# Kernel tuning notes

Measured on AMD Instinct MI355X. Metric: run time of the kernel, lower is better.

## Reference

```python
import jax, jax.numpy as jnp
import numpy as np

EPS = 1e-5

def maxpool2(x):
    # 2x2 max pool, stride 2, NCHW
    B, C, H, W = x.shape
    return x.reshape(B, C, H // 2, 2, W // 2, 2).max(axis=(3, 5))

def conv1x1(x, w, b):
    # x: [B,C,H,W], w: [O,C], b: [O]
    return jnp.einsum('bchw,oc->bohw', x, w) + b[None, :, None, None]

def setup_inputs() -> dict:
    key = jax.random.key(0)
    ks = jax.random.split(key, 12)
    B, C, IC, H, W = 8, 256, 128, 128, 128
    s = 0.05
    return {
        'rgb': jax.random.normal(ks[0], (B, C, H, W), jnp.float32),
        'event': jax.random.normal(ks[1], (B, C, H, W), jnp.float32),
        'g_w': jax.random.normal(ks[2], (IC, C), jnp.float32) * s,
        'g_b': jax.random.normal(ks[3], (IC,), jnp.float32) * s,
        'theta_w': jax.random.normal(ks[4], (IC, C), jnp.float32) * s,
        'theta_b': jax.random.normal(ks[5], (IC,), jnp.float32) * s,
        'phi_w': jax.random.normal(ks[6], (IC, C), jnp.float32) * s,
        'phi_b': jax.random.normal(ks[7], (IC,), jnp.float32) * s,
        'W_w': jax.random.normal(ks[8], (C, IC), jnp.float32) * s,
        'W_b': jax.random.normal(ks[9], (C,), jnp.float32) * s,
        'bn_gamma': jax.random.normal(ks[10], (C,), jnp.float32) * s + 1.0,
        'bn_beta': jax.random.normal(ks[11], (C,), jnp.float32) * s,
    }

def reference(rgb, event, g_w, g_b, theta_w, theta_b, phi_w, phi_b, W_w, W_b, bn_gamma, bn_beta):
    B = rgb.shape[0]
    IC = g_w.shape[0]
    # initial shared 2x2 max pool on both modalities
    rgb_p = maxpool2(rgb)      # [B,C,h2,w2]
    ev_p = maxpool2(event)
    h2, w2 = rgb_p.shape[2], rgb_p.shape[3]
    # projections; g and phi have an extra sub_sample pool
    g_x = maxpool2(conv1x1(ev_p, g_w, g_b)).reshape(B, IC, -1)      # [B,IC,Nkv]
    g_x = jnp.swapaxes(g_x, 1, 2)                                    # [B,Nkv,IC]
    theta_x = conv1x1(rgb_p, theta_w, theta_b).reshape(B, IC, -1)    # [B,IC,Nq]
    theta_x = jnp.swapaxes(theta_x, 1, 2)                            # [B,Nq,IC]
    phi_x = maxpool2(conv1x1(ev_p, phi_w, phi_b)).reshape(B, IC, -1) # [B,IC,Nkv]
    # full attention: scores -> softmax -> value matmul
    f = jnp.einsum('bqc,bck->bqk', theta_x, phi_x)                   # [B,Nq,Nkv]
    f_div_C = jax.nn.softmax(f, axis=-1)
    y = jnp.einsum('bqk,bkc->bqc', f_div_C, g_x)                     # [B,Nq,IC]
    y = jnp.swapaxes(y, 1, 2).reshape(B, IC, h2, w2)
    # output 1x1 conv + BatchNorm (training-mode batch stats, biased var)
    W_y = conv1x1(y, W_w, W_b)                                       # [B,C,h2,w2]
    mean = W_y.mean(axis=(0, 2, 3), keepdims=True)
    var = W_y.var(axis=(0, 2, 3), keepdims=True)
    W_y = (W_y - mean) * jax.lax.rsqrt(var + EPS)
    W_y = W_y * bn_gamma[None, :, None, None] + bn_beta[None, :, None, None]
    z = W_y + rgb_p
    z = jnp.repeat(jnp.repeat(z, 2, axis=2), 2, axis=3)
    return z
```

## Files before the change

### kernel.cpp

```cpp
#include <hip/hip_runtime.h>
#include <stdint.h>


typedef unsigned short u16;
typedef short bf16x8 __attribute__((ext_vector_type(8)));
typedef float f32x4 __attribute__((ext_vector_type(4)));

#define MFMA16(a, b, c) __builtin_amdgcn_mfma_f32_16x16x32_bf16(a, b, c, 0, 0, 0)

__device__ __forceinline__ u16 f2bf(float x) {
    union { float f; unsigned int u; } v; v.f = x;
    unsigned int u = v.u;
    unsigned int r = u + 0x7fffu + ((u >> 16) & 1u);
    return (u16)(r >> 16);
}
__device__ __forceinline__ float bf2f(u16 h) {
    union { unsigned int u; float f; } v; v.u = ((unsigned int)h) << 16;
    return v.f;
}

__global__ void wsplit_kernel(const float* __restrict__ tw, const float* __restrict__ pw,
                              const float* __restrict__ gw, const float* __restrict__ ww,
                              u16* __restrict__ planes, float* __restrict__ acc) {
    if (blockIdx.x == 0) {
        acc[threadIdx.x] = 0.0f;
        acc[256 + threadIdx.x] = 0.0f;
    }
    int idx = blockIdx.x * 256 + threadIdx.x;
    int m = idx >> 15, p = idx & 32767;
    const float* src = (m == 0) ? tw : (m == 1) ? pw : (m == 2) ? gw : ww;
    int se;
    if (m < 3) {
        int e = p & 7, lane = (p >> 3) & 63, kc = (p >> 9) & 7, ocb = p >> 12;
        int l16 = lane & 15, quad = lane >> 4;
        se = (ocb * 16 + l16) * 256 + kc * 32 + quad * 8 + e;
    } else {
        se = p;
    }
    float v = src[se];
    u16 h = f2bf(v);
    planes[m * 65536 + p] = h;
    planes[m * 65536 + 32768 + p] = f2bf(v - bf2f(h));
}

__global__ __launch_bounds__(512) void fused_pool_conv_kernel(
    const float* __restrict__ xr, const float* __restrict__ xe,
    const u16* __restrict__ Th, const u16* __restrict__ Tl, const float* __restrict__ tb,
    const u16* __restrict__ Fh, const u16* __restrict__ Fl, const float* __restrict__ fb,
    const u16* __restrict__ Gh, const float* __restrict__ gb,
    u16* __restrict__ th_o, u16* __restrict__ tl_o,
    u16* __restrict__ fh_o, u16* __restrict__ fl_o,
    u16* __restrict__ g_o, u16* __restrict__ pool_hi) {
    __shared__ u16 Ph[64 * 256];
    __shared__ u16 Plo[64 * 256];

    int bx = blockIdx.x;
    bool ev = bx >= 512;
    int bxx = bx & 511;
    int b = bxx >> 6, h2 = bxx & 63;
    int tid = threadIdx.x;
    int lane = tid & 63, quad = lane >> 4, l16 = lane & 15;
    int w = tid >> 6, mhalf = w & 1, nq = w >> 1;

    const float* x = ev ? xe : xr;
    const u16* W1h = ev ? Fh : Th;
    const u16* W1l = ev ? Fl : Tl;
    const float* b1 = ev ? fb : tb;
    u16* o1_hi = ev ? fh_o : th_o;
    u16* o1_lo = ev ? fl_o : tl_o;

    bf16x8 wh[2][2], wl[2][2], wg[2][2];
#pragma unroll
    for (int nt = 0; nt < 2; nt++) {
        long wo = ((long)((nq * 2 + nt) * 8 + 0) * 64 + lane) * 8;
        wh[0][nt] = *(const bf16x8*)&W1h[wo];
        wl[0][nt] = *(const bf16x8*)&W1l[wo];
        if (ev) wg[0][nt] = *(const bf16x8*)&Gh[wo];
    }

    long ibase = (long)b * 256 * 16384 + (long)(2 * h2) * 128;
    int coff = (bx * 37) & 255;
#pragma unroll 8
    for (int i = 0; i < 16; i++) {
        int u = i * 512 + tid;
        int c0 = u >> 5, w4 = u & 31;
        int c = (c0 + coff) & 255;
        const float* p = &x[ibase + (long)c * 16384 + w4 * 4];
        float4 r0 = *(const float4*)p;
        float4 r1 = *(const float4*)(p + 128);
        float p0 = fmaxf(fmaxf(r0.x, r0.y), fmaxf(r1.x, r1.y));
        float p1 = fmaxf(fmaxf(r0.z, r0.w), fmaxf(r1.z, r1.w));
        int row0 = 2 * w4, row1 = row0 + 1;
        int g = c >> 3, e = c & 7;
        u16 h0 = f2bf(p0), l0 = f2bf(p0 - bf2f(h0));
        u16 h1 = f2bf(p1), l1 = f2bf(p1 - bf2f(h1));
        int o0 = row0 * 256 + (((g ^ (row0 & 31)) << 3) | e);
        int o1 = row1 * 256 + (((g ^ (row1 & 31)) << 3) | e);
        Ph[o0] = h0; Plo[o0] = l0;
        Ph[o1] = h1; Plo[o1] = l1;
    }
    __syncthreads();

    f32x4 a1[2][2];
    f32x4 a2[2][2];
#pragma unroll
    for (int mt = 0; mt < 2; mt++)
#pragma unroll
        for (int nt = 0; nt < 2; nt++) {
#pragma unroll
            for (int r = 0; r < 4; r++) a1[mt][nt][r] = 0.0f;
#pragma unroll
            for (int r = 0; r < 4; r++) a2[mt][nt][r] = 0.0f;
        }

#pragma unroll
    for (int kc = 0; kc < 8; kc++) {
        int cur = kc & 1, nxt = cur ^ 1;
        if (kc < 7) {
#pragma unroll
            for (int nt = 0; nt < 2; nt++) {
                long wo = ((long)((nq * 2 + nt) * 8 + (kc + 1)) * 64 + lane) * 8;
                wh[nxt][nt] = *(const bf16x8*)&W1h[wo];
                wl[nxt][nt] = *(const bf16x8*)&W1l[wo];
                if (ev) wg[nxt][nt] = *(const bf16x8*)&Gh[wo];
            }
        }
        bf16x8 ah[2], al[2];
#pragma unroll
        for (int mt = 0; mt < 2; mt++) {
            int arow = mhalf * 32 + mt * 16 + l16;
            int g = kc * 4 + quad;
            int off = arow * 256 + ((g ^ (arow & 31)) << 3);
            ah[mt] = *(const bf16x8*)&Ph[off];
            al[mt] = *(const bf16x8*)&Plo[off];
        }
#pragma unroll
        for (int mt = 0; mt < 2; mt++)
#pragma unroll
            for (int nt = 0; nt < 2; nt++) {
                a1[mt][nt] = MFMA16(ah[mt], wh[cur][nt], a1[mt][nt]);
                a1[mt][nt] = MFMA16(ah[mt], wl[cur][nt], a1[mt][nt]);
                a1[mt][nt] = MFMA16(al[mt], wh[cur][nt], a1[mt][nt]);
                if (ev) a2[mt][nt] = MFMA16(ah[mt], wg[cur][nt], a2[mt][nt]);
            }
    }

    long mbase = (long)b * 4096 + h2 * 64;
#pragma unroll
    for (int mt = 0; mt < 2; mt++)
#pragma unroll
        for (int nt = 0; nt < 2; nt++) {
            int colo = nq * 32 + nt * 16 + l16;
            float bv1 = b1[colo];
            float bv2 = ev ? gb[colo] : 0.0f;
#pragma unroll
            for (int r = 0; r < 4; r++) {
                long row = mbase + mhalf * 32 + mt * 16 + quad * 4 + r;
                long idx = row * 128 + colo;
                float v = a1[mt][nt][r] + bv1;
                u16 h = f2bf(v);
                o1_hi[idx] = h;
                o1_lo[idx] = f2bf(v - bf2f(h));
                if (ev) g_o[idx] = f2bf(a2[mt][nt][r] + bv2);
            }
        }

    if (!ev) {
#pragma unroll 4
        for (int i = 0; i < 16; i++) {
            int r = i * 4 + (tid >> 7);
            int c = (tid & 127) * 2;
            int g = c >> 3;
            ushort2 hh = *(const ushort2*)&Ph[r * 256 + (((g ^ (r & 31)) << 3) | (c & 7))];
            *(ushort2*)&pool_hi[(mbase + r) * 256 + c] = hh;
        }
    }
}

__global__ __launch_bounds__(256) void pool_mid_kernel(
    const u16* __restrict__ fhi, const u16* __restrict__ flo,
    u16* __restrict__ khi, u16* __restrict__ klo,
    const u16* __restrict__ gsrc, u16* __restrict__ vt) {
    __shared__ u16 t[64][65];
    int bX = blockIdx.x;
    int tid = threadIdx.x;
    if (bX < 512) {
        int idx = bX * 256 + tid;
        int c8 = (idx & 15) * 8;
        int kv = (idx >> 4) & 1023;
        int b = idx >> 14;
        int h4 = kv >> 5, w4 = kv & 31;
        long p00 = ((long)b * 4096 + (2 * h4) * 64 + 2 * w4) * 128 + c8;
        bf16x8 h0 = *(const bf16x8*)&fhi[p00];
        bf16x8 h1 = *(const bf16x8*)&fhi[p00 + 128];
        bf16x8 h2 = *(const bf16x8*)&fhi[p00 + 8192];
        bf16x8 h3 = *(const bf16x8*)&fhi[p00 + 8320];
        bf16x8 l0 = *(const bf16x8*)&flo[p00];
        bf16x8 l1 = *(const bf16x8*)&flo[p00 + 128];
        bf16x8 l2 = *(const bf16x8*)&flo[p00 + 8192];
        bf16x8 l3 = *(const bf16x8*)&flo[p00 + 8320];
        bf16x8 oh, ol;
#pragma unroll
        for (int e = 0; e < 8; e++) {
            float v = fmaxf(fmaxf(bf2f((u16)h0[e]) + bf2f((u16)l0[e]),
                                  bf2f((u16)h1[e]) + bf2f((u16)l1[e])),
                            fmaxf(bf2f((u16)h2[e]) + bf2f((u16)l2[e]),
                                  bf2f((u16)h3[e]) + bf2f((u16)l3[e])));
            u16 h = f2bf(v);
            oh[e] = (short)h;
            ol[e] = (short)f2bf(v - bf2f(h));
        }
        long oi = ((long)b * 1024 + kv) * 128 + c8;
        *(bf16x8*)&khi[oi] = oh;
        *(bf16x8*)&klo[oi] = ol;
    } else {
        int bx = bX - 512;
        int ct = bx & 1, kvt = (bx >> 1) & 15, b = bx >> 5;
#pragma unroll 4
        for (int i = 0; i < 16; i++) {
            int idx = i * 256 + tid;
            int kv_l = idx >> 6, c_l = idx & 63;
            int kv = kvt * 64 + kv_l;
            int h4 = kv >> 5, w4 = kv & 31;
            long p00 = ((long)b * 4096 + (2 * h4) * 64 + 2 * w4) * 128 + ct * 64 + c_l;
            float v = fmaxf(fmaxf(bf2f(gsrc[p00]), bf2f(gsrc[p00 + 128])),
                            fmaxf(bf2f(gsrc[p00 + 8192]), bf2f(gsrc[p00 + 8192 + 128])));
            t[c_l][kv_l] = f2bf(v);
        }
        __syncthreads();
        long ob = ((long)b * 128 + ct * 64) * 1024 + kvt * 64;
#pragma unroll 4
        for (int i = 0; i < 16; i++) {
            int idx = i * 256 + tid;
            int c_l = idx >> 6, kv_l = idx & 63;
            vt[ob + (long)c_l * 1024 + kv_l] = t[c_l][kv_l];
        }
    }
}

__global__ __launch_bounds__(512, 4) void attn_kernel(
    const u16* __restrict__ th, const u16* __restrict__ tl,
    const u16* __restrict__ khi, const u16* __restrict__ klo,
    const u16* __restrict__ vt, u16* __restrict__ y) {
    __shared__ u16 Kh[2][32][136];
    __shared__ u16 Kl[2][32][136];
    __shared__ u16 Vt[2][128][40];
    __shared__ u16 Pl[8][16][40];

    int bx = blockIdx.x;
    int b = bx & 7, qt = bx >> 3;
    int tid = threadIdx.x;
    int w = tid >> 6, g = w >> 2, wsub = w & 3;
    int lane = tid & 63, quad = lane >> 4, l16 = lane & 15;
    int qbase = qt * 64 + wsub * 16;

    int krow = (tid >> 4) & 31, kko = (tid & 15) * 8;
    int vrow = (tid >> 2) & 127, vko = (tid & 3) * 8;
    long kb0 = ((long)b * 1024 + krow) * 128 + kko;
    long vb0 = ((long)b * 128 + vrow) * 1024 + vko;
    uint4 rkh0, rkh1, rkl0, rkl1, rv0, rv1;

#define STAGE_LOAD(IT) do {                                   \
        long k0 = kb0 + (long)(IT) * 4096;                    \
        rkh0 = *(const uint4*)&khi[k0];                       \
        rkl0 = *(const uint4*)&klo[k0];                       \
        rkh1 = *(const uint4*)&khi[k0 + 65536];               \
        rkl1 = *(const uint4*)&klo[k0 + 65536];               \
        long v0 = vb0 + (IT) * 32;                            \
        rv0 = *(const uint4*)&vt[v0];                         \
        rv1 = *(const uint4*)&vt[v0 + 512];                   \
    } while (0)

#define STAGE_WRITE() do {                                    \
        *(uint4*)&Kh[0][krow][kko] = rkh0;                    \
        *(uint4*)&Kl[0][krow][kko] = rkl0;                    \
        *(uint4*)&Kh[1][krow][kko] = rkh1;                    \
        *(uint4*)&Kl[1][krow][kko] = rkl1;                    \
        *(uint4*)&Vt[0][vrow][vko] = rv0;                     \
        *(uint4*)&Vt[1][vrow][vko] = rv1;                     \
    } while (0)

    bf16x8 qh[4], ql[4];
    long tb = ((long)b * 4096 + qbase + l16) * 128;
#pragma unroll
    for (int kc = 0; kc < 4; kc++) {
        qh[kc] = *(const bf16x8*)&th[tb + kc * 32 + quad * 8];
        ql[kc] = *(const bf16x8*)&tl[tb + kc * 32 + quad * 8];
    }

    f32x4 o[8];
#pragma unroll
    for (int t2 = 0; t2 < 8; t2++)
#pragma unroll
        for (int r = 0; r < 4; r++) o[t2][r] = 0.0f;
    float lp[4] = {0.0f, 0.0f, 0.0f, 0.0f};

    STAGE_LOAD(0);
    STAGE_WRITE();
    __syncthreads();
    STAGE_LOAD(1);

#pragma unroll 1
    for (int it = 0; it < 16; it++) {
        f32x4 s[2];
#pragma unroll
        for (int nt = 0; nt < 2; nt++)
#pragma unroll
            for (int r = 0; r < 4; r++) s[nt][r] = 0.0f;
#pragma unroll
        for (int kc = 0; kc < 4; kc++) {
#pragma unroll
            for (int nt = 0; nt < 2; nt++) {
                bf16x8 bh = *(const bf16x8*)&Kh[g][nt * 16 + l16][kc * 32 + quad * 8];
                bf16x8 bl = *(const bf16x8*)&Kl[g][nt * 16 + l16][kc * 32 + quad * 8];
                s[nt] = MFMA16(qh[kc], bh, s[nt]);
                s[nt] = MFMA16(qh[kc], bl, s[nt]);
                s[nt] = MFMA16(ql[kc], bh, s[nt]);
            }
        }

#pragma unroll
        for (int nt = 0; nt < 2; nt++)
#pragma unroll
            for (int r = 0; r < 4; r++) {
                float p = __expf(s[nt][r]);
                lp[r] += p;
                Pl[w][quad * 4 + r][nt * 16 + l16] = f2bf(p);
            }

        bf16x8 pa = *(const bf16x8*)&Pl[w][l16][quad * 8];
#pragma unroll
        for (int t2 = 0; t2 < 8; t2++) {
            bf16x8 vb = *(const bf16x8*)&Vt[g][t2 * 16 + l16][quad * 8];
            o[t2] = MFMA16(pa, vb, o[t2]);
        }

        __syncthreads();
        if (it < 15) {
            STAGE_WRITE();
            __syncthreads();
            if (it < 14) STAGE_LOAD(it + 2);
        }
    }

#pragma unroll
    for (int r = 0; r < 4; r++)
#pragma unroll
        for (int off = 1; off < 16; off <<= 1) lp[r] += __shfl_xor(lp[r], off);

    __syncthreads();
    float* Ob = (float*)&Kh[0][0][0];
    float* Lb = (float*)&Vt[0][0][0];
    if (g == 1) {
#pragma unroll
        for (int t2 = 0; t2 < 8; t2++)
#pragma unroll
            for (int r = 0; r < 4; r++)
                Ob[(wsub * 16 + quad * 4 + r) * 132 + t2 * 16 + l16] = o[t2][r];
        if (l16 == 0)
#pragma unroll
            for (int r = 0; r < 4; r++) Lb[wsub * 16 + quad * 4 + r] = lp[r];
    }
    __syncthreads();
    if (g == 0) {
#pragma unroll
        for (int r = 0; r < 4; r++) {
            int lrow = wsub * 16 + quad * 4 + r;
            float inv = 1.0f / (lp[r] + Lb[lrow]);
            long row = (long)b * 4096 + qbase + quad * 4 + r;
#pragma unroll
            for (int t2 = 0; t2 < 8; t2++) {
                float ov = o[t2][r] + Ob[lrow * 132 + t2 * 16 + l16];
                y[row * 128 + t2 * 16 + l16] = f2bf(ov * inv);
            }
        }
    }
#undef STAGE_LOAD
#undef STAGE_WRITE
}

__global__ __launch_bounds__(256) void wconv_kernel(
    const u16* __restrict__ A, const u16* __restrict__ Wh,
    const float* __restrict__ bias, float* __restrict__ out_f,
    float* __restrict__ acc_g) {
    __shared__ float red[4][2][256];
    int tid = threadIdx.x;
    int wave = tid >> 6, lane = tid & 63, quad = lane >> 4, l16 = lane & 15;
    long mbase = (long)blockIdx.x * 64 + wave * 16;

    f32x4 acc[16];
#pragma unroll
    for (int nt = 0; nt < 16; nt++)
#pragma unroll
        for (int r = 0; r < 4; r++) acc[nt][r] = 0.0f;

#pragma unroll
    for (int kc = 0; kc < 4; kc++) {
        bf16x8 ah = *(const bf16x8*)&A[(mbase + l16) * 128 + kc * 32 + quad * 8];
#pragma unroll
        for (int nt = 0; nt < 16; nt++) {
            bf16x8 bh = *(const bf16x8*)&Wh[(long)(nt * 16 + l16) * 128 + kc * 32 + quad * 8];
            acc[nt] = MFMA16(ah, bh, acc[nt]);
        }
    }

#pragma unroll
    for (int nt = 0; nt < 16; nt++) {
        int colo = nt * 16 + l16;
        float bv = bias[colo];
        float vs = 0.0f, vq = 0.0f;
#pragma unroll
        for (int r = 0; r < 4; r++) {
            long row = mbase + quad * 4 + r;
            float v = acc[nt][r] + bv;
            out_f[row * 256 + colo] = v;
            vs += v;
            vq += v * v;
        }
        vs += __shfl_xor(vs, 16); vs += __shfl_xor(vs, 32);
        vq += __shfl_xor(vq, 16); vq += __shfl_xor(vq, 32);
        if (quad == 0) {
            red[wave][0][colo] = vs;
            red[wave][1][colo] = vq;
        }
    }
    __syncthreads();
    if (tid < 256) {
        int c = tid;
        float s = red[0][0][c] + red[1][0][c] + red[2][0][c] + red[3][0][c];
        float q = red[0][1][c] + red[1][1][c] + red[2][1][c] + red[3][1][c];
        atomicAdd(&acc_g[c], s);
        atomicAdd(&acc_g[256 + c], q);
    }
}

__global__ __launch_bounds__(256) void final_kernel(
    const float* __restrict__ wy, const u16* __restrict__ rgbhi,
    const float* __restrict__ acc, const float* __restrict__ gamma,
    const float* __restrict__ beta, float* __restrict__ out) {
    __shared__ float z[16][257];
    int bx = blockIdx.x;
    int wt = bx & 3, h2 = (bx >> 2) & 63, b = bx >> 8;
    int c = threadIdx.x;

    float mean = acc[c] * (1.0f / 32768.0f);
    float var = acc[256 + c] * (1.0f / 32768.0f) - mean * mean;
    float rstd = rsqrtf(var + 1e-5f);
    float gm = gamma[c] * rstd;
    float bt = beta[c] - mean * gm;

    long pbase = (long)b * 4096 + h2 * 64 + wt * 16;
#pragma unroll 4
    for (int i = 0; i < 16; i++) {
        long pi = (pbase + i) * 256 + c;
        z[i][c] = wy[pi] * gm + bt + bf2f(rgbhi[pi]);
    }
    __syncthreads();

    int tid = threadIdx.x;
    int w8 = tid & 7, cg = tid >> 3;
#pragma unroll
    for (int it = 0; it < 8; it++) {
        int cc = it * 32 + cg;
        float za = z[2 * w8][cc];
        float zb = z[2 * w8 + 1][cc];
        float4 v = make_float4(za, za, zb, zb);
        long rowb = (((long)b * 256 + cc) * 128 + 2 * h2) * 128 + wt * 32 + w8 * 4;
        *(float4*)&out[rowb] = v;
        *(float4*)&out[rowb + 128] = v;
    }
}

extern "C" void kernel_launch(void* const* d_in, const int* in_sizes, int n_in,
                              void* d_out, int out_size, void* d_ws, size_t ws_size,
                              hipStream_t stream) {
    const float* rgb     = (const float*)d_in[0];
    const float* event_  = (const float*)d_in[1];
    const float* g_w     = (const float*)d_in[2];
    const float* g_b     = (const float*)d_in[3];
    const float* theta_w = (const float*)d_in[4];
    const float* theta_b = (const float*)d_in[5];
    const float* phi_w   = (const float*)d_in[6];
    const float* phi_b   = (const float*)d_in[7];
    const float* W_w     = (const float*)d_in[8];
    const float* W_b     = (const float*)d_in[9];
    const float* gamma   = (const float*)d_in[10];
    const float* beta    = (const float*)d_in[11];

    char* ws = (char*)d_ws;
    u16* rgbpt_hi = (u16*)(ws + 0);
    u16* theta_hi = (u16*)(ws + 16777216);
    u16* theta_lo = (u16*)(ws + 25165824);
    u16* phiF_hi  = (u16*)(ws + 33554432);
    u16* phiF_lo  = (u16*)(ws + 41943040);
    u16* g_full   = (u16*)(ws + 50331648);
    u16* phiK_hi  = (u16*)(ws + 58720256);
    u16* phiK_lo  = (u16*)(ws + 60817408);
    u16* gVt      = (u16*)(ws + 62914560);
    u16* y        = (u16*)(ws + 65011712);
    float* Wy     = (float*)(ws + 73400320);
    u16* wplanes  = (u16*)(ws + 106954752);
    float* acc    = (float*)(ws + 107479040);

    wsplit_kernel<<<512, 256, 0, stream>>>(theta_w, phi_w, g_w, W_w, wplanes, acc);

    fused_pool_conv_kernel<<<1024, 512, 0, stream>>>(
        rgb, event_,
        wplanes + 0, wplanes + 32768, theta_b,
        wplanes + 65536, wplanes + 98304, phi_b,
        wplanes + 131072, g_b,
        theta_hi, theta_lo, phiF_hi, phiF_lo, g_full, rgbpt_hi);

    pool_mid_kernel<<<768, 256, 0, stream>>>(phiF_hi, phiF_lo, phiK_hi, phiK_lo,
                                             g_full, gVt);

    attn_kernel<<<512, 512, 0, stream>>>(theta_hi, theta_lo, phiK_hi, phiK_lo, gVt, y);

    wconv_kernel<<<512, 256, 0, stream>>>(y, wplanes + 196608, W_b, Wy, acc);

    final_kernel<<<2048, 256, 0, stream>>>(Wy, rgbpt_hi, acc, gamma, beta, (float*)d_out);
}
```

Measured before the change: 462.8 us.

## Recompute output conv in final kernel instead of storing fp32 Wy

The W projection GEMM output is no longer written to a 32 MB fp32 buffer. The first pass now only accumulates BatchNorm sums. The final kernel recomputes the small 128-deep GEMM from the bf16 y tile with MFMA, then applies normalization, the residual and the upsample. This removes one full fp32 write and read of Wy, at the cost of doing the GEMM twice and adding MFMA work to the store-bound final kernel.

```diff
diff --git a/kernel.cpp b/kernel.cpp
--- a/kernel.cpp
+++ b/kernel.cpp
@@ -379,10 +379,9 @@
 #undef STAGE_WRITE
 }
 
-__global__ __launch_bounds__(256) void wconv_kernel(
+__global__ __launch_bounds__(256) void wstats_kernel(
     const u16* __restrict__ A, const u16* __restrict__ Wh,
-    const float* __restrict__ bias, float* __restrict__ out_f,
-    float* __restrict__ acc_g) {
+    const float* __restrict__ bias, float* __restrict__ acc_g) {
     __shared__ float red[4][2][256];
     int tid = threadIdx.x;
     int wave = tid >> 6, lane = tid & 63, quad = lane >> 4, l16 = lane & 15;
@@ -411,9 +410,7 @@
         float vs = 0.0f, vq = 0.0f;
 #pragma unroll
         for (int r = 0; r < 4; r++) {
-            long row = mbase + quad * 4 + r;
             float v = acc[nt][r] + bv;
-            out_f[row * 256 + colo] = v;
             vs += v;
             vq += v * v;
         }
@@ -435,29 +432,55 @@
 }
 
 __global__ __launch_bounds__(256) void final_kernel(
-    const float* __restrict__ wy, const u16* __restrict__ rgbhi,
+    const u16* __restrict__ y, const u16* __restrict__ Wh,
+    const float* __restrict__ wb, const u16* __restrict__ rgbhi,
     const float* __restrict__ acc, const float* __restrict__ gamma,
     const float* __restrict__ beta, float* __restrict__ out) {
     __shared__ float z[16][257];
     int bx = blockIdx.x;
     int wt = bx & 3, h2 = (bx >> 2) & 63, b = bx >> 8;
-    int c = threadIdx.x;
-
-    float mean = acc[c] * (1.0f / 32768.0f);
-    float var = acc[256 + c] * (1.0f / 32768.0f) - mean * mean;
-    float rstd = rsqrtf(var + 1e-5f);
-    float gm = gamma[c] * rstd;
-    float bt = beta[c] - mean * gm;
-
+    int tid = threadIdx.x;
+    int w = tid >> 6, lane = tid & 63, quad = lane >> 4, l16 = lane & 15;
     long pbase = (long)b * 4096 + h2 * 64 + wt * 16;
-#pragma unroll 4
-    for (int i = 0; i < 16; i++) {
-        long pi = (pbase + i) * 256 + c;
-        z[i][c] = wy[pi] * gm + bt + bf2f(rgbhi[pi]);
+
+    bf16x8 ya[4];
+#pragma unroll
+    for (int kc = 0; kc < 4; kc++)
+        ya[kc] = *(const bf16x8*)&y[(pbase + l16) * 128 + kc * 32 + quad * 8];
+
+    f32x4 a[4];
+#pragma unroll
+    for (int nt = 0; nt < 4; nt++)
+#pragma unroll
+        for (int r = 0; r < 4; r++) a[nt][r] = 0.0f;
+
+#pragma unroll
+    for (int kc = 0; kc < 4; kc++)
+#pragma unroll
+        for (int nt = 0; nt < 4; nt++) {
+            int colo = w * 64 + nt * 16 + l16;
+            bf16x8 bh = *(const bf16x8*)&Wh[(long)colo * 128 + kc * 32 + quad * 8];
+            a[nt] = MFMA16(ya[kc], bh, a[nt]);
+        }
+
+#pragma unroll
+    for (int nt = 0; nt < 4; nt++) {
+        int colo = w * 64 + nt * 16 + l16;
+        float mean = acc[colo] * (1.0f / 32768.0f);
+        float var = acc[256 + colo] * (1.0f / 32768.0f) - mean * mean;
+        float rstd = rsqrtf(var + 1e-5f);
+        float gm = gamma[colo] * rstd;
+        float bt = beta[colo] - mean * gm;
+        float bv = wb[colo];
+#pragma unroll
+        for (int r = 0; r < 4; r++) {
+            int pos = quad * 4 + r;
+            float v = a[nt][r] + bv;
+            z[pos][colo] = v * gm + bt + bf2f(rgbhi[(pbase + pos) * 256 + colo]);
+        }
     }
     __syncthreads();
 
-    int tid = threadIdx.x;
     int w8 = tid & 7, cg = tid >> 3;
 #pragma unroll
     for (int it = 0; it < 8; it++) {
@@ -498,9 +521,8 @@
     u16* phiK_lo  = (u16*)(ws + 60817408);
     u16* gVt      = (u16*)(ws + 62914560);
     u16* y        = (u16*)(ws + 65011712);
-    float* Wy     = (float*)(ws + 73400320);
-    u16* wplanes  = (u16*)(ws + 106954752);
-    float* acc    = (float*)(ws + 107479040);
+    u16* wplanes  = (u16*)(ws + 73400320);
+    float* acc    = (float*)(ws + 73924608);
 
     wsplit_kernel<<<512, 256, 0, stream>>>(theta_w, phi_w, g_w, W_w, wplanes, acc);
 
@@ -516,7 +538,8 @@
 
     attn_kernel<<<512, 512, 0, stream>>>(theta_hi, theta_lo, phiK_hi, phiK_lo, gVt, y);
 
-    wconv_kernel<<<512, 256, 0, stream>>>(y, wplanes + 196608, W_b, Wy, acc);
-
-    final_kernel<<<2048, 256, 0, stream>>>(Wy, rgbpt_hi, acc, gamma, beta, (float*)d_out);
-}
+    wstats_kernel<<<512, 256, 0, stream>>>(y, wplanes + 196608, W_b, acc);
+
+    final_kernel<<<2048, 256, 0, stream>>>(y, wplanes + 196608, W_b, rgbpt_hi,
+                                           acc, gamma, beta, (float*)d_out);
+}
```

Result: no change. 461.4 us (-0.3%).
